# Kernel optimization log

Measured on AMD Instinct MI355X. Metric: run time of the kernel, lower is better.

## Reference

```python
import jax, jax.numpy as jnp
import numpy as np

N, E, F_IN, D, EF, L, G = 50000, 800000, 92, 64, 50, 3, 128
EPS = 1e-5


def setup_inputs() -> dict:
    key = jax.random.key(0)
    ks = jax.random.split(key, 16)
    Z = 2 * D + EF  # concat dim for CGConv messages
    inp = {
        "x": jax.random.normal(ks[0], (N, F_IN), dtype=jnp.float32),
        "edge_index": jax.random.randint(ks[1], (2, E), 0, N, dtype=jnp.int32),
        "edge_attr": jax.random.uniform(ks[2], (E, EF), dtype=jnp.float32),
        "batch": jnp.sort(jax.random.randint(ks[3], (N,), 0, G, dtype=jnp.int32)),
        "pre_W": jax.random.normal(ks[4], (F_IN, D), dtype=jnp.float32) * 0.05,
        "pre_b": jnp.zeros((D,), jnp.float32),
        "Wf": jax.random.normal(ks[5], (L, Z, D), dtype=jnp.float32) * 0.05,
        "bf": jnp.zeros((L, D), jnp.float32),
        "Ws": jax.random.normal(ks[6], (L, Z, D), dtype=jnp.float32) * 0.05,
        "bs": jnp.zeros((L, D), jnp.float32),
        "bn_gamma": jnp.ones((L, D), jnp.float32) + 0.1 * jax.random.normal(ks[7], (L, D), dtype=jnp.float32),
        "bn_beta": 0.1 * jax.random.normal(ks[8], (L, D), dtype=jnp.float32),
        "bn_mean": 0.1 * jax.random.normal(ks[9], (L, D), dtype=jnp.float32),
        "bn_var": jax.random.uniform(ks[10], (L, D), dtype=jnp.float32, minval=0.5, maxval=1.5),
        "post_W": jax.random.normal(ks[11], (D, D), dtype=jnp.float32) * 0.05,
        "post_b": jnp.zeros((D,), jnp.float32),
        "out_W": jax.random.normal(ks[12], (D, 1), dtype=jnp.float32) * 0.05,
        "out_b": jnp.zeros((1,), jnp.float32),
    }
    return inp


def reference(x, edge_index, edge_attr, batch, pre_W, pre_b, Wf, bf, Ws, bs,
              bn_gamma, bn_beta, bn_mean, bn_var, post_W, post_b, out_W, out_b):
    src = edge_index[0]  # x_j (source)
    dst = edge_index[1]  # x_i (target, aggregation index)

    # pre FC + relu
    h = jax.nn.relu(x @ pre_W + pre_b)

    # in-degree for mean aggregation
    deg = jax.ops.segment_sum(jnp.ones((E,), h.dtype), dst, num_segments=N)
    deg = jnp.maximum(deg, 1.0)[:, None]

    for l in range(L):
        # CGConv: z_ij = [h_i || h_j || e_ij]
        z = jnp.concatenate([h[dst], h[src], edge_attr], axis=-1)  # [E, 2D+EF]
        m = jax.nn.sigmoid(z @ Wf[l] + bf[l]) * jax.nn.softplus(z @ Ws[l] + bs[l])
        agg = jax.ops.segment_sum(m, dst, num_segments=N) / deg
        h = h + agg  # residual in CGConv
        # BatchNorm1d (eval mode, running stats); dropout is identity in eval
        h = bn_gamma[l] * (h - bn_mean[l]) * jax.lax.rsqrt(bn_var[l] + EPS) + bn_beta[l]

    # early global_mean_pool over graphs
    cnt = jax.ops.segment_sum(jnp.ones((N,), h.dtype), batch, num_segments=G)
    cnt = jnp.maximum(cnt, 1.0)[:, None]
    g = jax.ops.segment_sum(h, batch, num_segments=G) / cnt  # [G, D]

    g = jax.nn.relu(g @ post_W + post_b)
    return g @ out_W + out_b  # [G, 1]
```

## Files before the change

### kernel.cpp

```cpp
#include <hip/hip_runtime.h>
#include <cmath>

#define N_NODES 50000
#define N_EDGES 800000
#define F_IN 92
#define DIM 64
#define EF 50
#define NLAYER 3
#define NGRAPH 128
#define ZROWS 178

using short8 = __attribute__((ext_vector_type(8))) short;
using f32x4  = __attribute__((ext_vector_type(4))) float;

__device__ __forceinline__ unsigned short f2bf(float v) {
    unsigned int u = __float_as_uint(v);
    return (unsigned short)((u + 0x7FFFu + ((u >> 16) & 1u)) >> 16);
}
__device__ __forceinline__ float bf2f(unsigned short h) {
    return __uint_as_float(((unsigned int)h) << 16);
}

__global__ __launch_bounds__(256, 3) void pre_fc(const float* __restrict__ x,
                                                 const float* __restrict__ W,
                                                 const float* __restrict__ b,
                                                 float* __restrict__ h,
                                                 unsigned short* __restrict__ hh,
                                                 unsigned short* __restrict__ hl, int N)
{
    const int lane = threadIdx.x & 63;
    const int wid  = blockIdx.x * (blockDim.x >> 6) + (threadIdx.x >> 6);
    const int nw   = gridDim.x * (blockDim.x >> 6);
    float w[F_IN];
#pragma unroll
    for (int k = 0; k < F_IN; ++k) w[k] = W[k * DIM + lane];
    const float bb = b[lane];
#pragma unroll 1
    for (int n = wid; n < N; n += nw) {
        const int nu = __builtin_amdgcn_readfirstlane(n);
        const float* xr = x + (size_t)nu * F_IN;
        float a = bb;
#pragma unroll
        for (int k = 0; k < F_IN; ++k) a = fmaf(xr[k], w[k], a);
        const float rv = fmaxf(a, 0.f);
        const size_t idx = (size_t)nu * DIM + lane;
        h[idx] = rv;
        const unsigned short hb = f2bf(rv);
        hh[idx] = hb;
        hl[idx] = f2bf(rv - bf2f(hb));
    }
}

__global__ __launch_bounds__(256) void deg_cnt(const int* __restrict__ ei, int E,
                                               const int* __restrict__ batch, int N,
                                               float* __restrict__ deg,
                                               float* __restrict__ cnt)
{
    const int i = blockIdx.x * blockDim.x + threadIdx.x;
    const int stride = gridDim.x * blockDim.x;
    for (int e = i; e < E; e += stride) unsafeAtomicAdd(&deg[ei[E + e]], 1.f);
    for (int n = i; n < N; n += stride) unsafeAtomicAdd(&cnt[batch[n]], 1.f);
}

__global__ __launch_bounds__(256) void prep_wsplit(const float* __restrict__ Wf,
                                                   const float* __restrict__ Ws,
                                                   unsigned short* __restrict__ Wth,
                                                   unsigned short* __restrict__ Wtl)
{
    const int i = blockIdx.x * blockDim.x + threadIdx.x;
    if (i >= NLAYER * 128 * 64) return;
    const int l = i >> 13;
    const int rem = i & 8191;
    const int c = rem >> 6;
    const int k = rem & 63;
    float v = 0.f;
    if (k < EF) {
        const size_t base = (size_t)l * ZROWS * DIM + (size_t)(2 * DIM + k) * DIM;
        v = (c < 64) ? Wf[base + c] : Ws[base + (c - 64)];
    }
    const unsigned short hb = f2bf(v);
    Wth[i] = hb;
    Wtl[i] = f2bf(v - bf2f(hb));
}

__global__ __launch_bounds__(256) void prep_nwsplit(const float* __restrict__ Wf,
                                                    const float* __restrict__ Ws,
                                                    const float* __restrict__ bf,
                                                    const float* __restrict__ bs,
                                                    unsigned short* __restrict__ Wnh,
                                                    unsigned short* __restrict__ Wnl,
                                                    float* __restrict__ pbias)
{
    const int i = blockIdx.x * blockDim.x + threadIdx.x;
    if (i >= NLAYER * 256 * 64) return;
    const int l = i >> 14;
    const int rem = i & 16383;
    const int c = rem >> 6;
    const int k = rem & 63;
    const size_t lb = (size_t)l * ZROWS * DIM;
    float v;
    if (c < 64)       v = Wf[lb + (size_t)k * DIM + c];
    else if (c < 128) v = Ws[lb + (size_t)k * DIM + (c - 64)];
    else if (c < 192) v = Wf[lb + (size_t)(64 + k) * DIM + (c - 128)];
    else              v = Ws[lb + (size_t)(64 + k) * DIM + (c - 192)];
    const unsigned short hb = f2bf(v);
    Wnh[i] = hb;
    Wnl[i] = f2bf(v - bf2f(hb));
    if (k == 0)
        pbias[l * 256 + c] = (c < 64) ? bf[l * DIM + c]
                           : ((c < 128) ? bs[l * DIM + (c - 64)] : 0.f);
}

#define HS_STR 72
__global__ __launch_bounds__(512) void node_proj_mfma(
    const unsigned short* __restrict__ hh,
    const unsigned short* __restrict__ hl,
    const unsigned short* __restrict__ Wnh,
    const unsigned short* __restrict__ Wnl,
    const float* __restrict__ pbias,
    float* __restrict__ Pd, float* __restrict__ Ps, int N)
{
    __shared__ unsigned short lh[64 * HS_STR];
    __shared__ unsigned short ll[64 * HS_STR];
    const int tid = threadIdx.x;
    const int n0 = blockIdx.x * 64;

    {
        const int row = tid >> 3, c8 = tid & 7;
        const int n = n0 + row;
        short8 hv = (short8){0,0,0,0,0,0,0,0};
        short8 lv = (short8){0,0,0,0,0,0,0,0};
        if (n < N) {
            const size_t gs = (size_t)n * 64 + c8 * 8;
            hv = *reinterpret_cast<const short8*>(hh + gs);
            lv = *reinterpret_cast<const short8*>(hl + gs);
        }
        *reinterpret_cast<short8*>(lh + row * HS_STR + c8 * 8) = hv;
        *reinterpret_cast<short8*>(ll + row * HS_STR + c8 * 8) = lv;
    }
    __syncthreads();

    const int l  = tid & 63;
    const int wv = __builtin_amdgcn_readfirstlane(tid >> 6);
    const int mt = wv & 3, ng = wv >> 2;
    const int r = l & 15, g = l >> 4;
    const int arow = mt * 16 + r;

    short8 ah[2], al[2];
#pragma unroll
    for (int kc = 0; kc < 2; ++kc) {
        const int off = arow * HS_STR + kc * 32 + g * 8;
        ah[kc] = *reinterpret_cast<const short8*>(lh + off);
        al[kc] = *reinterpret_cast<const short8*>(ll + off);
    }

    f32x4 acc[8];
#pragma unroll
    for (int nt = 0; nt < 8; ++nt) acc[nt] = (f32x4){0.f, 0.f, 0.f, 0.f};

#pragma unroll
    for (int nt = 0; nt < 8; ++nt) {
        const int col = ng * 128 + nt * 16 + r;
        const unsigned short* bp = Wnh + (size_t)col * 64 + g * 8;
        const unsigned short* lp = Wnl + (size_t)col * 64 + g * 8;
#pragma unroll
        for (int kc = 0; kc < 2; ++kc) {
            const short8 bh = *reinterpret_cast<const short8*>(bp + kc * 32);
            const short8 bl = *reinterpret_cast<const short8*>(lp + kc * 32);
            acc[nt] = __builtin_amdgcn_mfma_f32_16x16x32_bf16(ah[kc], bh, acc[nt], 0, 0, 0);
            acc[nt] = __builtin_amdgcn_mfma_f32_16x16x32_bf16(ah[kc], bl, acc[nt], 0, 0, 0);
            acc[nt] = __builtin_amdgcn_mfma_f32_16x16x32_bf16(al[kc], bh, acc[nt], 0, 0, 0);
        }
    }

    float* P = ng ? Ps : Pd;
#pragma unroll
    for (int nt = 0; nt < 8; ++nt) {
        const int c = nt * 16 + r;
        const float bias = ng ? 0.f : pbias[c];
#pragma unroll
        for (int rr = 0; rr < 4; ++rr) {
            const int n = n0 + mt * 16 + g * 4 + rr;
            if (n < N) P[(size_t)n * 128 + c] = acc[nt][rr] + bias;
        }
    }
}

#define EA_STR 72
__global__ __launch_bounds__(512) void edge_fused(const int* __restrict__ ei,
                                                  const float* __restrict__ eattr,
                                                  const float* __restrict__ Pd,
                                                  const float* __restrict__ Ps,
                                                  const unsigned short* __restrict__ Wth,
                                                  const unsigned short* __restrict__ Wtl,
                                                  float* __restrict__ agg, int E)
{
    __shared__ unsigned short lds_h[128 * EA_STR];
    __shared__ unsigned short lds_l[128 * EA_STR];

    const int tid = threadIdx.x;
    const int e0  = blockIdx.x * 128;

#pragma unroll
    for (int it = 0; it < 2; ++it) {
        const int u = tid + it * 512;
        const int row = u >> 3;
        const int c8  = u & 7;
        const float* er = eattr + (size_t)(e0 + row) * EF;
        short8 hv, lv;
#pragma unroll
        for (int j = 0; j < 8; ++j) {
            const int k = c8 * 8 + j;
            const float v = (k < EF) ? er[k] : 0.f;
            const unsigned short hb = f2bf(v);
            hv[j] = (short)hb;
            lv[j] = (short)f2bf(v - bf2f(hb));
        }
        *reinterpret_cast<short8*>(lds_h + row * EA_STR + c8 * 8) = hv;
        *reinterpret_cast<short8*>(lds_l + row * EA_STR + c8 * 8) = lv;
    }
    __syncthreads();

    const int l  = tid & 63;
    const int wv = __builtin_amdgcn_readfirstlane(tid >> 6);
    const int r  = l & 15;
    const int g  = l >> 4;
    const int rbase = wv * 16;

    short8 ah[2], al[2];
#pragma unroll
    for (int kc = 0; kc < 2; ++kc) {
        const int off = (rbase + r) * EA_STR + kc * 32 + g * 8;
        ah[kc] = *reinterpret_cast<const short8*>(lds_h + off);
        al[kc] = *reinterpret_cast<const short8*>(lds_l + off);
    }

    f32x4 acc[8];
#pragma unroll
    for (int nt = 0; nt < 8; ++nt) acc[nt] = (f32x4){0.f, 0.f, 0.f, 0.f};
#pragma unroll
    for (int nt = 0; nt < 8; ++nt) {
        const int col = nt * 16 + r;
        const unsigned short* bp = Wth + (size_t)col * 64 + g * 8;
        const unsigned short* lp = Wtl + (size_t)col * 64 + g * 8;
#pragma unroll
        for (int kc = 0; kc < 2; ++kc) {
            const short8 bh = *reinterpret_cast<const short8*>(bp + kc * 32);
            const short8 bl = *reinterpret_cast<const short8*>(lp + kc * 32);
            acc[nt] = __builtin_amdgcn_mfma_f32_16x16x32_bf16(ah[kc], bh, acc[nt], 0, 0, 0);
            acc[nt] = __builtin_amdgcn_mfma_f32_16x16x32_bf16(ah[kc], bl, acc[nt], 0, 0, 0);
            acc[nt] = __builtin_amdgcn_mfma_f32_16x16x32_bf16(al[kc], bh, acc[nt], 0, 0, 0);
        }
    }

#pragma unroll
    for (int rr = 0; rr < 4; ++rr) {
        const int eg = e0 + rbase + g * 4 + rr;
        const int dd = ei[E + eg];
        const int ss = ei[eg];
        const float* pdr = Pd + (size_t)dd * 128 + r;
        const float* psr = Ps + (size_t)ss * 128 + r;
        float pdv[8], psv[8];
#pragma unroll
        for (int nt = 0; nt < 8; ++nt) {
            pdv[nt] = pdr[nt * 16];
            psv[nt] = psr[nt * 16];
        }
        float* ag = agg + (size_t)dd * DIM + r;
#pragma unroll
        for (int nt = 0; nt < 4; ++nt) {
            const float zf = acc[nt][rr]     + pdv[nt]     + psv[nt];
            const float zs = acc[nt + 4][rr] + pdv[nt + 4] + psv[nt + 4];
            const float sig = 1.f / (1.f + __expf(-zf));
            const float sp  = fmaxf(zs, 0.f) + __logf(1.f + __expf(-fabsf(zs)));
            unsafeAtomicAdd(ag + nt * 16, sig * sp);
        }
    }
}

__global__ __launch_bounds__(256) void node_update(float* __restrict__ h,
                                                   unsigned short* __restrict__ hh,
                                                   unsigned short* __restrict__ hl,
                                                   const float* __restrict__ agg,
                                                   const float* __restrict__ deg,
                                                   const float* __restrict__ gamma,
                                                   const float* __restrict__ beta,
                                                   const float* __restrict__ mean,
                                                   const float* __restrict__ var, int N)
{
    const int lane = threadIdx.x & 63;
    const float g  = gamma[lane];
    const float bt = beta[lane];
    const float mn = mean[lane];
    const float iv = rsqrtf(var[lane] + 1e-5f);
    const int idx = blockIdx.x * blockDim.x + threadIdx.x;
    const int stride = gridDim.x * blockDim.x;
    const int total = N * DIM;
    for (int i = idx; i < total; i += stride) {
        const int n = i >> 6;
        const float inv = 1.f / fmaxf(deg[n], 1.f);
        const float v = h[i] + agg[i] * inv;
        const float rv = fmaf(g, (v - mn) * iv, bt);
        h[i] = rv;
        const unsigned short hb = f2bf(rv);
        hh[i] = hb;
        hl[i] = f2bf(rv - bf2f(hb));
    }
}

__global__ __launch_bounds__(256) void pool_sum(const float* __restrict__ h,
                                                const int* __restrict__ batch,
                                                float* __restrict__ gsum, int N)
{
    const int lane = threadIdx.x & 63;
    const int wid  = blockIdx.x * (blockDim.x >> 6) + (threadIdx.x >> 6);
    const int nw   = gridDim.x * (blockDim.x >> 6);
    for (int n = wid; n < N; n += nw) {
        const int nu = __builtin_amdgcn_readfirstlane(n);
        const int b = batch[nu];
        unsafeAtomicAdd(&gsum[(size_t)b * DIM + lane], h[(size_t)nu * DIM + lane]);
    }
}

__global__ __launch_bounds__(64) void head(const float* __restrict__ gsum,
                                           const float* __restrict__ cnt,
                                           const float* __restrict__ postW,
                                           const float* __restrict__ postb,
                                           const float* __restrict__ outW,
                                           const float* __restrict__ outb,
                                           float* __restrict__ out)
{
    const int gi = blockIdx.x;
    const int lane = threadIdx.x;
    const float inv = 1.f / fmaxf(cnt[gi], 1.f);
    const float gval = gsum[(size_t)gi * DIM + lane] * inv;
    float acc = postb[lane];
#pragma unroll
    for (int k = 0; k < DIM; ++k) acc = fmaf(__shfl(gval, k, 64), postW[k * DIM + lane], acc);
    const float t = fmaxf(acc, 0.f);
    float prod = t * outW[lane];
#pragma unroll
    for (int off = 32; off > 0; off >>= 1) prod += __shfl_down(prod, off, 64);
    if (lane == 0) out[gi] = prod + outb[0];
}

extern "C" void kernel_launch(void* const* d_in, const int* in_sizes, int n_in,
                              void* d_out, int out_size, void* d_ws, size_t ws_size,
                              hipStream_t stream)
{
    const float* x     = (const float*)d_in[0];
    const int*   ei    = (const int*)d_in[1];
    const float* eattr = (const float*)d_in[2];
    const int*   batch = (const int*)d_in[3];
    const float* preW  = (const float*)d_in[4];
    const float* preb  = (const float*)d_in[5];
    const float* Wf    = (const float*)d_in[6];
    const float* bf    = (const float*)d_in[7];
    const float* Ws    = (const float*)d_in[8];
    const float* bs    = (const float*)d_in[9];
    const float* gamma = (const float*)d_in[10];
    const float* beta  = (const float*)d_in[11];
    const float* mean  = (const float*)d_in[12];
    const float* var   = (const float*)d_in[13];
    const float* postW = (const float*)d_in[14];
    const float* postb = (const float*)d_in[15];
    const float* outW  = (const float*)d_in[16];
    const float* outb  = (const float*)d_in[17];
    float* out = (float*)d_out;

    const int N = N_NODES, E = N_EDGES, G = NGRAPH;

    char* p = (char*)d_ws;
    unsigned short* hh = (unsigned short*)p; p += (size_t)N * DIM * 2;
    unsigned short* hl = (unsigned short*)p; p += (size_t)N * DIM * 2;
    float* h      = (float*)p; p += (size_t)N * DIM * 4;
    float* Pd     = (float*)p; p += (size_t)N * 128 * 4;
    float* Ps     = (float*)p; p += (size_t)N * 128 * 4;
    float* agg    = (float*)p; p += (size_t)N * DIM * 4;
    float* gsum   = (float*)p; p += (size_t)G * DIM * 4;
    float* cnt    = (float*)p; p += (size_t)G * 4;
    float* deg    = (float*)p; p += (size_t)N * 4;
    unsigned short* Wth = (unsigned short*)p; p += (size_t)NLAYER * 128 * 64 * 2;
    unsigned short* Wtl = (unsigned short*)p; p += (size_t)NLAYER * 128 * 64 * 2;
    unsigned short* Wnh = (unsigned short*)p; p += (size_t)NLAYER * 256 * 64 * 2;
    unsigned short* Wnl = (unsigned short*)p; p += (size_t)NLAYER * 256 * 64 * 2;
    float* pbias  = (float*)p; p += (size_t)NLAYER * 256 * 4;

    hipMemsetAsync(gsum, 0, ((size_t)G * DIM + G + N) * 4, stream);

    deg_cnt<<<512, 256, 0, stream>>>(ei, E, batch, N, deg, cnt);
    prep_wsplit<<<(NLAYER * 128 * 64 + 255) / 256, 256, 0, stream>>>(Wf, Ws, Wth, Wtl);
    prep_nwsplit<<<(NLAYER * 256 * 64 + 255) / 256, 256, 0, stream>>>(Wf, Ws, bf, bs,
                                                                      Wnh, Wnl, pbias);

    pre_fc<<<512, 256, 0, stream>>>(x, preW, preb, h, hh, hl, N);

    const int nblk = (N + 63) / 64;
    for (int l = 0; l < NLAYER; ++l) {
        hipMemsetAsync(agg, 0, (size_t)N * DIM * 4, stream);
        node_proj_mfma<<<nblk, 512, 0, stream>>>(hh, hl,
                                                 Wnh + (size_t)l * 16384,
                                                 Wnl + (size_t)l * 16384,
                                                 pbias + (size_t)l * 256, Pd, Ps, N);
        edge_fused<<<E / 128, 512, 0, stream>>>(ei, eattr, Pd, Ps,
                                                Wth + (size_t)l * 8192,
                                                Wtl + (size_t)l * 8192, agg, E);
        node_update<<<1024, 256, 0, stream>>>(h, hh, hl, agg, deg, gamma + l * DIM,
                                              beta + l * DIM, mean + l * DIM,
                                              var + l * DIM, N);
    }

    pool_sum<<<512, 256, 0, stream>>>(h, batch, gsum, N);
    head<<<G, 64, 0, stream>>>(gsum, cnt, postW, postb, outW, outb, out);
}
```

Measured before the change: 1.278 ms.

## Replace bf16-split MFMA edge projection with fp32 FMA and coalesced gathers

The edge-attribute projection now runs in plain fp32 FMAs on edge attributes staged in LDS, instead of a three-pass bf16 hi/lo split MFMA, so the prep_wsplit kernel and per-edge bf16 conversion go away. Results are written to LDS, and a second phase gathers Pd/Ps rows with each lane reading one column, giving coalesced row loads and atomics. The bf16 split of h moves from pre_fc and node_update into node_proj_mfma, so the hh/hl buffers are no longer written. The trade is more scalar ALU work in the edge kernel (50x128 FMAs per edge, weights read from global), plus an extra LDS round trip and barrier.

```diff
diff --git a/kernel.cpp b/kernel.cpp
--- a/kernel.cpp
+++ b/kernel.cpp
@@ -24,9 +24,7 @@
 __global__ __launch_bounds__(256, 3) void pre_fc(const float* __restrict__ x,
                                                  const float* __restrict__ W,
                                                  const float* __restrict__ b,
-                                                 float* __restrict__ h,
-                                                 unsigned short* __restrict__ hh,
-                                                 unsigned short* __restrict__ hl, int N)
+                                                 float* __restrict__ h, int N)
 {
     const int lane = threadIdx.x & 63;
     const int wid  = blockIdx.x * (blockDim.x >> 6) + (threadIdx.x >> 6);
@@ -42,12 +40,7 @@
         float a = bb;
 #pragma unroll
         for (int k = 0; k < F_IN; ++k) a = fmaf(xr[k], w[k], a);
-        const float rv = fmaxf(a, 0.f);
-        const size_t idx = (size_t)nu * DIM + lane;
-        h[idx] = rv;
-        const unsigned short hb = f2bf(rv);
-        hh[idx] = hb;
-        hl[idx] = f2bf(rv - bf2f(hb));
+        h[(size_t)nu * DIM + lane] = fmaxf(a, 0.f);
     }
 }
 
@@ -60,27 +53,6 @@
     const int stride = gridDim.x * blockDim.x;
     for (int e = i; e < E; e += stride) unsafeAtomicAdd(&deg[ei[E + e]], 1.f);
     for (int n = i; n < N; n += stride) unsafeAtomicAdd(&cnt[batch[n]], 1.f);
-}
-
-__global__ __launch_bounds__(256) void prep_wsplit(const float* __restrict__ Wf,
-                                                   const float* __restrict__ Ws,
-                                                   unsigned short* __restrict__ Wth,
-                                                   unsigned short* __restrict__ Wtl)
-{
-    const int i = blockIdx.x * blockDim.x + threadIdx.x;
-    if (i >= NLAYER * 128 * 64) return;
-    const int l = i >> 13;
-    const int rem = i & 8191;
-    const int c = rem >> 6;
-    const int k = rem & 63;
-    float v = 0.f;
-    if (k < EF) {
-        const size_t base = (size_t)l * ZROWS * DIM + (size_t)(2 * DIM + k) * DIM;
-        v = (c < 64) ? Wf[base + c] : Ws[base + (c - 64)];
-    }
-    const unsigned short hb = f2bf(v);
-    Wth[i] = hb;
-    Wtl[i] = f2bf(v - bf2f(hb));
 }
 
 __global__ __launch_bounds__(256) void prep_nwsplit(const float* __restrict__ Wf,
@@ -113,8 +85,7 @@
 
 #define HS_STR 72
 __global__ __launch_bounds__(512) void node_proj_mfma(
-    const unsigned short* __restrict__ hh,
-    const unsigned short* __restrict__ hl,
+    const float* __restrict__ h,
     const unsigned short* __restrict__ Wnh,
     const unsigned short* __restrict__ Wnl,
     const float* __restrict__ pbias,
@@ -131,9 +102,14 @@
         short8 hv = (short8){0,0,0,0,0,0,0,0};
         short8 lv = (short8){0,0,0,0,0,0,0,0};
         if (n < N) {
-            const size_t gs = (size_t)n * 64 + c8 * 8;
-            hv = *reinterpret_cast<const short8*>(hh + gs);
-            lv = *reinterpret_cast<const short8*>(hl + gs);
+            const float* hr = h + (size_t)n * DIM + c8 * 8;
+#pragma unroll
+            for (int j = 0; j < 8; ++j) {
+                const float v = hr[j];
+                const unsigned short hb = f2bf(v);
+                hv[j] = (short)hb;
+                lv[j] = (short)f2bf(v - bf2f(hb));
+            }
         }
         *reinterpret_cast<short8*>(lh + row * HS_STR + c8 * 8) = hv;
         *reinterpret_cast<short8*>(ll + row * HS_STR + c8 * 8) = lv;
@@ -186,101 +162,89 @@
     }
 }
 
-#define EA_STR 72
+#define EA_PAD 51
+#define TP_PAD 129
 __global__ __launch_bounds__(512) void edge_fused(const int* __restrict__ ei,
                                                   const float* __restrict__ eattr,
                                                   const float* __restrict__ Pd,
                                                   const float* __restrict__ Ps,
-                                                  const unsigned short* __restrict__ Wth,
-                                                  const unsigned short* __restrict__ Wtl,
+                                                  const float* __restrict__ WfE,
+                                                  const float* __restrict__ WsE,
                                                   float* __restrict__ agg, int E)
 {
-    __shared__ unsigned short lds_h[128 * EA_STR];
-    __shared__ unsigned short lds_l[128 * EA_STR];
+    __shared__ float ea_lds[64 * EA_PAD];
+    __shared__ float out_lds[64 * TP_PAD];
 
     const int tid = threadIdx.x;
-    const int e0  = blockIdx.x * 128;
-
-#pragma unroll
-    for (int it = 0; it < 2; ++it) {
-        const int u = tid + it * 512;
-        const int row = u >> 3;
-        const int c8  = u & 7;
-        const float* er = eattr + (size_t)(e0 + row) * EF;
-        short8 hv, lv;
-#pragma unroll
-        for (int j = 0; j < 8; ++j) {
-            const int k = c8 * 8 + j;
-            const float v = (k < EF) ? er[k] : 0.f;
-            const unsigned short hb = f2bf(v);
-            hv[j] = (short)hb;
-            lv[j] = (short)f2bf(v - bf2f(hb));
-        }
-        *reinterpret_cast<short8*>(lds_h + row * EA_STR + c8 * 8) = hv;
-        *reinterpret_cast<short8*>(lds_l + row * EA_STR + c8 * 8) = lv;
+    const int e0  = blockIdx.x * 64;
+
+    {
+        const float* src = eattr + (size_t)e0 * EF;
+        for (int idx = tid; idx < 64 * EF; idx += 512) {
+            const int e = idx / EF;
+            const int k = idx - e * EF;
+            ea_lds[e * EA_PAD + k] = src[idx];
+        }
     }
     __syncthreads();
 
-    const int l  = tid & 63;
-    const int wv = __builtin_amdgcn_readfirstlane(tid >> 6);
-    const int r  = l & 15;
-    const int g  = l >> 4;
-    const int rbase = wv * 16;
-
-    short8 ah[2], al[2];
-#pragma unroll
-    for (int kc = 0; kc < 2; ++kc) {
-        const int off = (rbase + r) * EA_STR + kc * 32 + g * 8;
-        ah[kc] = *reinterpret_cast<const short8*>(lds_h + off);
-        al[kc] = *reinterpret_cast<const short8*>(lds_l + off);
-    }
-
-    f32x4 acc[8];
-#pragma unroll
-    for (int nt = 0; nt < 8; ++nt) acc[nt] = (f32x4){0.f, 0.f, 0.f, 0.f};
-#pragma unroll
-    for (int nt = 0; nt < 8; ++nt) {
-        const int col = nt * 16 + r;
-        const unsigned short* bp = Wth + (size_t)col * 64 + g * 8;
-        const unsigned short* lp = Wtl + (size_t)col * 64 + g * 8;
-#pragma unroll
-        for (int kc = 0; kc < 2; ++kc) {
-            const short8 bh = *reinterpret_cast<const short8*>(bp + kc * 32);
-            const short8 bl = *reinterpret_cast<const short8*>(lp + kc * 32);
-            acc[nt] = __builtin_amdgcn_mfma_f32_16x16x32_bf16(ah[kc], bh, acc[nt], 0, 0, 0);
-            acc[nt] = __builtin_amdgcn_mfma_f32_16x16x32_bf16(ah[kc], bl, acc[nt], 0, 0, 0);
-            acc[nt] = __builtin_amdgcn_mfma_f32_16x16x32_bf16(al[kc], bh, acc[nt], 0, 0, 0);
-        }
-    }
-
-#pragma unroll
-    for (int rr = 0; rr < 4; ++rr) {
-        const int eg = e0 + rbase + g * 4 + rr;
-        const int dd = ei[E + eg];
-        const int ss = ei[eg];
-        const float* pdr = Pd + (size_t)dd * 128 + r;
-        const float* psr = Ps + (size_t)ss * 128 + r;
-        float pdv[8], psv[8];
-#pragma unroll
-        for (int nt = 0; nt < 8; ++nt) {
-            pdv[nt] = pdr[nt * 16];
-            psv[nt] = psr[nt * 16];
-        }
-        float* ag = agg + (size_t)dd * DIM + r;
-#pragma unroll
-        for (int nt = 0; nt < 4; ++nt) {
-            const float zf = acc[nt][rr]     + pdv[nt]     + psv[nt];
-            const float zs = acc[nt + 4][rr] + pdv[nt + 4] + psv[nt + 4];
+    {
+        const int e  = tid & 63;
+        const int wv = __builtin_amdgcn_readfirstlane(tid >> 6);
+        const float* Wbase = (wv < 4) ? WfE : WsE;
+        const int c0 = (wv & 3) * 16;
+        const int cb = ((wv < 4) ? 0 : 64) + c0;
+
+        float acc[16];
+#pragma unroll
+        for (int j = 0; j < 16; ++j) acc[j] = 0.f;
+
+        const float* ear = ea_lds + e * EA_PAD;
+#pragma unroll 5
+        for (int k = 0; k < EF; ++k) {
+            const float eak = ear[k];
+            const float* wr = Wbase + k * DIM + c0;
+#pragma unroll
+            for (int j = 0; j < 16; ++j) acc[j] = fmaf(eak, wr[j], acc[j]);
+        }
+        float* orow = out_lds + e * TP_PAD + cb;
+#pragma unroll
+        for (int j = 0; j < 16; ++j) orow[j] = acc[j];
+    }
+    __syncthreads();
+
+    {
+        const int lane = tid & 63;
+        const int wv   = __builtin_amdgcn_readfirstlane(tid >> 6);
+        const int base = e0 + wv * 8;
+
+        int dd[8], ss[8];
+#pragma unroll
+        for (int i = 0; i < 8; ++i) {
+            dd[i] = ei[E + base + i];
+            ss[i] = ei[base + i];
+        }
+        float pd0[8], pd1[8], ps0[8], ps1[8];
+#pragma unroll
+        for (int i = 0; i < 8; ++i) {
+            const float* pdr = Pd + (size_t)dd[i] * 128;
+            const float* psr = Ps + (size_t)ss[i] * 128;
+            pd0[i] = pdr[lane]; pd1[i] = pdr[64 + lane];
+            ps0[i] = psr[lane]; ps1[i] = psr[64 + lane];
+        }
+#pragma unroll
+        for (int i = 0; i < 8; ++i) {
+            const int el = wv * 8 + i;
+            const float zf = out_lds[el * TP_PAD + lane]      + pd0[i] + ps0[i];
+            const float zs = out_lds[el * TP_PAD + 64 + lane] + pd1[i] + ps1[i];
             const float sig = 1.f / (1.f + __expf(-zf));
             const float sp  = fmaxf(zs, 0.f) + __logf(1.f + __expf(-fabsf(zs)));
-            unsafeAtomicAdd(ag + nt * 16, sig * sp);
+            unsafeAtomicAdd(&agg[(size_t)dd[i] * DIM + lane], sig * sp);
         }
     }
 }
 
 __global__ __launch_bounds__(256) void node_update(float* __restrict__ h,
-                                                   unsigned short* __restrict__ hh,
-                                                   unsigned short* __restrict__ hl,
                                                    const float* __restrict__ agg,
                                                    const float* __restrict__ deg,
                                                    const float* __restrict__ gamma,
@@ -300,11 +264,7 @@
         const int n = i >> 6;
         const float inv = 1.f / fmaxf(deg[n], 1.f);
         const float v = h[i] + agg[i] * inv;
-        const float rv = fmaf(g, (v - mn) * iv, bt);
-        h[i] = rv;
-        const unsigned short hb = f2bf(rv);
-        hh[i] = hb;
-        hl[i] = f2bf(rv - bf2f(hb));
+        h[i] = fmaf(g, (v - mn) * iv, bt);
     }
 }
 
@@ -371,8 +331,6 @@
     const int N = N_NODES, E = N_EDGES, G = NGRAPH;
 
     char* p = (char*)d_ws;
-    unsigned short* hh = (unsigned short*)p; p += (size_t)N * DIM * 2;
-    unsigned short* hl = (unsigned short*)p; p += (size_t)N * DIM * 2;
     float* h      = (float*)p; p += (size_t)N * DIM * 4;
     float* Pd     = (float*)p; p += (size_t)N * 128 * 4;
     float* Ps     = (float*)p; p += (size_t)N * 128 * 4;
@@ -380,8 +338,6 @@
     float* gsum   = (float*)p; p += (size_t)G * DIM * 4;
     float* cnt    = (float*)p; p += (size_t)G * 4;
     float* deg    = (float*)p; p += (size_t)N * 4;
-    unsigned short* Wth = (unsigned short*)p; p += (size_t)NLAYER * 128 * 64 * 2;
-    unsigned short* Wtl = (unsigned short*)p; p += (size_t)NLAYER * 128 * 64 * 2;
     unsigned short* Wnh = (unsigned short*)p; p += (size_t)NLAYER * 256 * 64 * 2;
     unsigned short* Wnl = (unsigned short*)p; p += (size_t)NLAYER * 256 * 64 * 2;
     float* pbias  = (float*)p; p += (size_t)NLAYER * 256 * 4;
@@ -389,25 +345,25 @@
     hipMemsetAsync(gsum, 0, ((size_t)G * DIM + G + N) * 4, stream);
 
     deg_cnt<<<512, 256, 0, stream>>>(ei, E, batch, N, deg, cnt);
-    prep_wsplit<<<(NLAYER * 128 * 64 + 255) / 256, 256, 0, stream>>>(Wf, Ws, Wth, Wtl);
     prep_nwsplit<<<(NLAYER * 256 * 64 + 255) / 256, 256, 0, stream>>>(Wf, Ws, bf, bs,
                                                                       Wnh, Wnl, pbias);
 
-    pre_fc<<<512, 256, 0, stream>>>(x, preW, preb, h, hh, hl, N);
+    pre_fc<<<512, 256, 0, stream>>>(x, preW, preb, h, N);
 
     const int nblk = (N + 63) / 64;
     for (int l = 0; l < NLAYER; ++l) {
+        const float* Wfl = Wf + (size_t)l * ZROWS * DIM;
+        const float* Wsl = Ws + (size_t)l * ZROWS * DIM;
         hipMemsetAsync(agg, 0, (size_t)N * DIM * 4, stream);
-        node_proj_mfma<<<nblk, 512, 0, stream>>>(hh, hl,
+        node_proj_mfma<<<nblk, 512, 0, stream>>>(h,
                                                  Wnh + (size_t)l * 16384,
                                                  Wnl + (size_t)l * 16384,
                                                  pbias + (size_t)l * 256, Pd, Ps, N);
-        edge_fused<<<E / 128, 512, 0, stream>>>(ei, eattr, Pd, Ps,
-                                                Wth + (size_t)l * 8192,
-                                                Wtl + (size_t)l * 8192, agg, E);
-        node_update<<<1024, 256, 0, stream>>>(h, hh, hl, agg, deg, gamma + l * DIM,
-                                              beta + l * DIM, mean + l * DIM,
-                                              var + l * DIM, N);
+        edge_fused<<<E / 64, 512, 0, stream>>>(ei, eattr, Pd, Ps,
+                                               Wfl + 2 * DIM * DIM, Wsl + 2 * DIM * DIM,
+                                               agg, E);
+        node_update<<<1024, 256, 0, stream>>>(h, agg, deg, gamma + l * DIM, beta + l * DIM,
+                                              mean + l * DIM, var + l * DIM, N);
     }
 
     pool_sum<<<512, 256, 0, stream>>>(h, batch, gsum, N);
```

Result: faster. 1.095 ms (-14.3%).
